# Kernel tuning notes

Hardware: AMD Instinct MI355X
Metric: run time of the kernel (lower is better)

Reference implementation:

```python
import jax, jax.numpy as jnp
import numpy as np

B, S, D, NB = 8, 8192, 512, 16


def _ln(x, g, b, eps=1e-5):
    m = jnp.mean(x, axis=-1, keepdims=True)
    v = jnp.var(x, axis=-1, keepdims=True)
    return (x - m) / jnp.sqrt(v + eps) * g + b


def setup_inputs() -> dict:
    key = jax.random.key(0)
    ks = jax.random.split(key, 12)
    s = 0.02
    f32 = jnp.float32
    return {
        "emb_input": jax.random.normal(ks[0], (B, S, D), f32),
        "dis_input": jax.random.normal(ks[1], (B, S, D), f32),
        "torsion": jax.random.normal(ks[2], (B, D), f32),
        "dis_unlocked": 1,
        "delay_steps": 3,
        # embodied selector + per-block params (stacked over NB blocks)
        "emb_sel_W": jax.random.normal(ks[3], (D, NB), f32) * s,
        "emb_sel_b": jnp.zeros((NB,), f32),
        "emb_ln_g": jnp.ones((NB, D), f32),
        "emb_ln_b": jnp.zeros((NB, D), f32),
        "emb_w1": jax.random.normal(ks[4], (NB, D, D), f32) * s,
        "emb_b1": jnp.zeros((NB, D), f32),
        "emb_w2": jax.random.normal(ks[5], (NB, D, D), f32) * s,
        "emb_b2": jnp.zeros((NB, D), f32),
        # disembodied selector + per-block params
        "dis_sel_W": jax.random.normal(ks[6], (D, NB), f32) * s,
        "dis_sel_b": jnp.zeros((NB,), f32),
        "dis_ln1_g": jnp.ones((NB, D), f32),
        "dis_ln1_b": jnp.zeros((NB, D), f32),
        "dis_attn_W": jax.random.normal(ks[7], (NB, D, D), f32) * s,
        "dis_attn_b": jnp.zeros((NB, D), f32),
        "dis_ln2_g": jnp.ones((NB, D), f32),
        "dis_ln2_b": jnp.zeros((NB, D), f32),
        "dis_ff1_W": jax.random.normal(ks[8], (NB, D, 2 * D), f32) * s,
        "dis_ff1_b": jnp.zeros((NB, 2 * D), f32),
        "dis_ff2_W": jax.random.normal(ks[9], (NB, 2 * D, D), f32) * s,
        "dis_ff2_b": jnp.zeros((NB, D), f32),
    }


def reference(emb_input, dis_input, torsion, dis_unlocked, delay_steps,
              emb_sel_W, emb_sel_b, emb_ln_g, emb_ln_b, emb_w1, emb_b1, emb_w2, emb_b2,
              dis_sel_W, dis_sel_b, dis_ln1_g, dis_ln1_b, dis_attn_W, dis_attn_b,
              dis_ln2_g, dis_ln2_b, dis_ff1_W, dis_ff1_b, dis_ff2_W, dis_ff2_b):
    # ---- embodied branch: sigmoid-gated top-2 routing (indices from batch elem 0)
    scores = jax.nn.sigmoid(jnp.mean(emb_input, axis=1) @ emb_sel_W + emb_sel_b)  # [B,NB]
    _, top = jax.lax.top_k(scores[0], 2)
    t_emb = 1.0 + torsion[:, None, :] * 0.1  # [B,1,D]
    h = emb_input
    for i in range(2):  # fixed top-2, unrolled; block params gathered dynamically
        idx = top[i]
        hn = _ln(h, emb_ln_g[idx], emb_ln_b[idx])
        hn = jnp.tanh(hn @ emb_w1[idx] + emb_b1[idx]) @ emb_w2[idx] + emb_b2[idx]
        h = h + hn * t_emb * 0.3
    emb_h = h

    # ---- disembodied branch (dis_unlocked is a static Python int)
    dis_h = None
    if dis_unlocked:
        delayed = jnp.mean(dis_input, axis=1)  # [B,D]; single-write buffer returns current mean
        dscores = jax.nn.sigmoid(delayed @ dis_sel_W + dis_sel_b)
        _, dtop = jax.lax.top_k(dscores[0], 2)
        t_dis = 1.0 + torsion[:, None, :] * 0.05
        dh = dis_input
        for i in range(2):
            idx = dtop[i]
            h1 = _ln(dh, dis_ln1_g[idx], dis_ln1_b[idx])
            h1 = h1 @ dis_attn_W[idx] + dis_attn_b[idx]
            h1 = (h1 + delayed[:, None, :] * 0.2) * t_dis
            hm = dh + h1 * 0.5
            h2 = _ln(hm, dis_ln2_g[idx], dis_ln2_b[idx])
            h2 = jax.nn.gelu(h2 @ dis_ff1_W[idx] + dis_ff1_b[idx], approximate=False)
            h2 = h2 @ dis_ff2_W[idx] + dis_ff2_b[idx]
            dh = hm + h2 * 0.5
        dis_h = dh
    return (emb_h, dis_h)
```

## Files before the change

kernel.cpp:

```cpp
#include <hip/hip_runtime.h>
#include <stdint.h>

#define B_  8
#define S_  8192
#define D_  512
#define NB_ 16
#define M_  (B_*S_)

typedef short bf16x8 __attribute__((ext_vector_type(8)));
typedef float f32x4  __attribute__((ext_vector_type(4)));

static __device__ __forceinline__ unsigned short f2bf(float f) {
  unsigned int u = __float_as_uint(f);
  u += 0x7fff + ((u >> 16) & 1);
  return (unsigned short)(u >> 16);
}

static __device__ __forceinline__ float fast_gelu(float v) {
  float x = fabsf(v) * 0.70710678118654752f;
  float t = __builtin_amdgcn_rcpf(1.f + 0.3275911f * x);
  float poly = ((((1.061405429f * t - 1.453152027f) * t + 1.421413741f) * t
                 - 0.284496736f) * t + 0.254829592f) * t;
  float erfx = 1.f - poly * __expf(-x * x);
  return 0.5f * v * (1.f + copysignf(erfx, v));
}

static __device__ __forceinline__ float fast_tanh(float v) {
  float a = fabsf(v);
  float e = __expf(2.f * a);
  float r = 1.f - 2.f * __builtin_amdgcn_rcpf(e + 1.f);
  return copysignf(r, v);
}

static __device__ __forceinline__ void async_copy16(const unsigned short* g,
                                                    unsigned short* l) {
  auto* g1 = reinterpret_cast<const __attribute__((address_space(1))) uint32_t*>(
      reinterpret_cast<uintptr_t>(g));
  auto* l3 = reinterpret_cast<__attribute__((address_space(3))) uint32_t*>(
      reinterpret_cast<uintptr_t>(l));
  __builtin_amdgcn_global_load_lds(g1, l3, 16, 0, 0);
}

__global__ __launch_bounds__(256) void zero_kernel(float* p, int n) {
  int i = blockIdx.x * 256 + threadIdx.x;
  if (i < n) p[i] = 0.f;
}

__global__ __launch_bounds__(512) void colmean_kernel(const float* __restrict__ x,
                                                      float* __restrict__ acc) {
  int b = blockIdx.x, d = threadIdx.x;
  const float* p = x + ((size_t)b * S_ + (size_t)blockIdx.y * 512) * D_ + d;
  float s = 0.f;
  #pragma unroll 8
  for (int i = 0; i < 512; i++) s += p[(size_t)i * D_];
  atomicAdd(&acc[b * D_ + d], s);
}

__global__ __launch_bounds__(128) void top2_kernel(const float* __restrict__ embAcc,
                                                   const float* __restrict__ embW,
                                                   const float* __restrict__ embB,
                                                   const float* __restrict__ disAcc,
                                                   const float* __restrict__ disW,
                                                   const float* __restrict__ disB,
                                                   int* __restrict__ out) {
  int wave = threadIdx.x >> 6, lane = threadIdx.x & 63;
  const float* acc = wave ? disAcc : embAcc;
  const float* W   = wave ? disW   : embW;
  const float* bb  = wave ? disB   : embB;
  const float invS = 1.f / (float)S_;
  float logit[NB_];
  for (int nb = 0; nb < NB_; nb++) {
    float s = 0.f;
    for (int d = lane; d < D_; d += 64) s += acc[d] * invS * W[d * NB_ + nb];
    for (int o = 32; o; o >>= 1) s += __shfl_xor(s, o);
    logit[nb] = s + bb[nb];
  }
  if (lane == 0) {
    int i0 = 0;
    for (int i = 1; i < NB_; i++) if (logit[i] > logit[i0]) i0 = i;
    int i1 = (i0 == 0) ? 1 : 0;
    for (int i = 0; i < NB_; i++) if (i != i0 && logit[i] > logit[i1]) i1 = i;
    out[wave * 2 + 0] = i0;
    out[wave * 2 + 1] = i1;
  }
}

__global__ __launch_bounds__(256) void ln_cast_kernel(const float* __restrict__ x,
                                                      const float* __restrict__ gB,
                                                      const float* __restrict__ bB,
                                                      const int* __restrict__ idxPtr,
                                                      unsigned short* __restrict__ out) {
  int row  = blockIdx.x * 4 + (threadIdx.x >> 6);
  int lane = threadIdx.x & 63;
  const float4* xr = (const float4*)(x + (size_t)row * D_ + lane * 8);
  float4 v0 = xr[0], v1 = xr[1];
  float s  = v0.x + v0.y + v0.z + v0.w + v1.x + v1.y + v1.z + v1.w;
  float sq = v0.x*v0.x + v0.y*v0.y + v0.z*v0.z + v0.w*v0.w
           + v1.x*v1.x + v1.y*v1.y + v1.z*v1.z + v1.w*v1.w;
  for (int o = 32; o; o >>= 1) { s += __shfl_xor(s, o); sq += __shfl_xor(sq, o); }
  float mean = s * (1.f / D_);
  float var  = sq * (1.f / D_) - mean * mean;
  float rstd = rsqrtf(var + 1e-5f);
  int idx = *idxPtr;
  const float4* g4 = (const float4*)(gB + (size_t)idx * D_ + lane * 8);
  const float4* b4 = (const float4*)(bB + (size_t)idx * D_ + lane * 8);
  float4 g0 = g4[0], g1 = g4[1], c0 = b4[0], c1 = b4[1];
  float xv[8] = {v0.x, v0.y, v0.z, v0.w, v1.x, v1.y, v1.z, v1.w};
  float gv[8] = {g0.x, g0.y, g0.z, g0.w, g1.x, g1.y, g1.z, g1.w};
  float bv[8] = {c0.x, c0.y, c0.z, c0.w, c1.x, c1.y, c1.z, c1.w};
  unsigned short o8[8] __attribute__((aligned(16)));
  #pragma unroll
  for (int k = 0; k < 8; k++) o8[k] = f2bf((xv[k] - mean) * rstd * gv[k] + bv[k]);
  *(uint4*)(out + (size_t)row * D_ + lane * 8) = *(const uint4*)o8;
}

__global__ __launch_bounds__(256) void wconvert_kernel(const float* __restrict__ srcAll,
                                                       const int* __restrict__ idxPtr,
                                                       int K, int N,
                                                       unsigned short* __restrict__ dst) {
  __shared__ float t[32][33];
  int idx = *idxPtr;
  const float* src = srcAll + (size_t)idx * K * N;
  int k0 = blockIdx.y * 32, n0 = blockIdx.x * 32;
  int tid = threadIdx.x;
  int kl = tid >> 5, nl = tid & 31;
  #pragma unroll
  for (int r = 0; r < 4; r++)
    t[kl + r * 8][nl] = src[(size_t)(k0 + kl + r * 8) * N + n0 + nl];
  __syncthreads();
  #pragma unroll
  for (int r = 0; r < 4; r++)
    dst[(size_t)(n0 + kl + r * 8) * K + k0 + nl] = f2bf(t[nl][kl + r * 8]);
}

template<int EPI>
__global__ __launch_bounds__(256, 3) void gemm_kernel(const unsigned short* __restrict__ A,
                                                      const unsigned short* __restrict__ Bt,
                                                      int K, int N,
                                                      const int* __restrict__ idxPtr,
                                                      const float* __restrict__ biasBase,
                                                      const float* __restrict__ hin,
                                                      float* __restrict__ fout,
                                                      unsigned short* __restrict__ bout,
                                                      const float* __restrict__ torsion,
                                                      const float* __restrict__ dAcc) {
  __shared__ __align__(16) unsigned short lds[3][2][4096];
  const int tid  = threadIdx.x;
  const int wid  = tid >> 6, lane = tid & 63;
  const int quad = lane >> 4, l16 = lane & 15;
  const int wm = (wid >> 1) * 64, wn = (wid & 1) * 64;

  const int nT  = N >> 7;
  const int lgn = (nT == 4) ? 2 : 3;
  const int perX = gridDim.x >> 3;
  const int tile = ((int)blockIdx.x & 7) * perX + ((int)blockIdx.x >> 3);
  const int m0 = (tile >> lgn) << 7;
  const int n0 = (tile & (nT - 1)) << 7;

  const int srow = tid >> 2;
  const int scol = (((tid & 3) ^ ((tid >> 3) & 3)) * 8);
  const unsigned short* Ag0 = A  + (size_t)(m0 + srow) * K + scol;
  const unsigned short* Ag1 = Ag0 + (size_t)64 * K;
  const unsigned short* Bg0 = Bt + (size_t)(n0 + srow) * K + scol;
  const unsigned short* Bg1 = Bg0 + (size_t)64 * K;

  auto stage = [&](int kt, int slot) {
    async_copy16(Ag0 + (size_t)kt * 32, &lds[slot][0][tid * 8]);
    async_copy16(Ag1 + (size_t)kt * 32, &lds[slot][0][2048 + tid * 8]);
    async_copy16(Bg0 + (size_t)kt * 32, &lds[slot][1][tid * 8]);
    async_copy16(Bg1 + (size_t)kt * 32, &lds[slot][1][2048 + tid * 8]);
  };

  f32x4 acc[4][4] = {};
  const int nK = K >> 5;

  stage(0, 0);
  stage(1, 1);

  const int rsw  = (l16 >> 1) & 3;
  const int aoff = (wm + l16) * 32 + ((quad ^ rsw) * 8);
  const int boff = (wn + l16) * 32 + ((quad ^ rsw) * 8);

  for (int k = 0; k < nK; ++k) {
    const int cur = k % 3;
    const int nxt = (k + 2) % 3;
    const int kn  = (k + 2 < nK) ? (k + 2) : 0;
    stage(kn, nxt);
    asm volatile("s_waitcnt vmcnt(8)" ::: "memory");
    asm volatile("s_barrier" ::: "memory");

    const unsigned short* Ab = &lds[cur][0][aoff];
    const unsigned short* Bb = &lds[cur][1][boff];
    bf16x8 af[4], bfr[4];
    #pragma unroll
    for (int i = 0; i < 4; ++i) af[i]  = *(const bf16x8*)(Ab + i * 512);
    #pragma unroll
    for (int j = 0; j < 4; ++j) bfr[j] = *(const bf16x8*)(Bb + j * 512);
    __builtin_amdgcn_s_setprio(1);
    #pragma unroll
    for (int i = 0; i < 4; ++i)
      #pragma unroll
      for (int j = 0; j < 4; ++j)
        acc[i][j] = __builtin_amdgcn_mfma_f32_16x16x32_bf16(af[i], bfr[j], acc[i][j], 0, 0, 0);
    __builtin_amdgcn_s_setprio(0);
    asm volatile("s_barrier" ::: "memory");
  }

  const int idx = *idxPtr;
  const float* bias = biasBase + (size_t)idx * N;
  const float invS = 1.f / (float)S_;
  #pragma unroll
  for (int i = 0; i < 4; ++i) {
    int rowb = m0 + wm + i * 16 + quad * 4;
    #pragma unroll
    for (int j = 0; j < 4; ++j) {
      int col = n0 + wn + j * 16 + l16;
      float bc = bias[col];
      #pragma unroll
      for (int r = 0; r < 4; ++r) {
        int row = rowb + r;
        size_t off = (size_t)row * N + col;
        float v = acc[i][j][r] + bc;
        if constexpr (EPI == 0) {
          bout[off] = f2bf(fast_tanh(v));
        } else if constexpr (EPI == 1) {
          int b = row >> 13;
          float t = 1.f + 0.1f * torsion[b * D_ + col];
          fout[off] = hin[off] + v * t * 0.3f;
        } else if constexpr (EPI == 2) {
          int b = row >> 13;
          float t = 1.f + 0.05f * torsion[b * D_ + col];
          float h1 = (v + 0.2f * dAcc[b * D_ + col] * invS) * t;
          fout[off] = hin[off] + 0.5f * h1;
        } else if constexpr (EPI == 3) {
          bout[off] = f2bf(fast_gelu(v));
        } else {
          fout[off] = hin[off] + 0.5f * v;
        }
      }
    }
  }
  asm volatile("s_waitcnt vmcnt(0)" ::: "memory");
}

extern "C" void kernel_launch(void* const* d_in, const int* in_sizes, int n_in,
                              void* d_out, int out_size, void* d_ws, size_t ws_size,
                              hipStream_t stream) {
  const float* emb_input  = (const float*)d_in[0];
  const float* dis_input  = (const float*)d_in[1];
  const float* torsion    = (const float*)d_in[2];
  const float* emb_sel_W  = (const float*)d_in[5];
  const float* emb_sel_b  = (const float*)d_in[6];
  const float* emb_ln_g   = (const float*)d_in[7];
  const float* emb_ln_b   = (const float*)d_in[8];
  const float* emb_w1     = (const float*)d_in[9];
  const float* emb_b1     = (const float*)d_in[10];
  const float* emb_w2     = (const float*)d_in[11];
  const float* emb_b2     = (const float*)d_in[12];
  const float* dis_sel_W  = (const float*)d_in[13];
  const float* dis_sel_b  = (const float*)d_in[14];
  const float* dis_ln1_g  = (const float*)d_in[15];
  const float* dis_ln1_b  = (const float*)d_in[16];
  const float* dis_attn_W = (const float*)d_in[17];
  const float* dis_attn_b = (const float*)d_in[18];
  const float* dis_ln2_g  = (const float*)d_in[19];
  const float* dis_ln2_b  = (const float*)d_in[20];
  const float* dis_ff1_W  = (const float*)d_in[21];
  const float* dis_ff1_b  = (const float*)d_in[22];
  const float* dis_ff2_W  = (const float*)d_in[23];
  const float* dis_ff2_b  = (const float*)d_in[24];

  char* w = (char*)d_ws;
  float* accE = (float*)w;
  float* accD = (float*)(w + 16384);
  int*   top  = (int*)(w + 32768);
  size_t o = 33024;
  unsigned short* w1t   = (unsigned short*)(w + o); o += 524288;
  unsigned short* w2t   = (unsigned short*)(w + o); o += 524288;
  unsigned short* attnT = (unsigned short*)(w + o); o += 524288;
  unsigned short* ff1T  = (unsigned short*)(w + o); o += 1048576;
  unsigned short* ff2T  = (unsigned short*)(w + o); o += 1048576;
  unsigned short* Abuf  = (unsigned short*)(w + o); o += (size_t)M_ * D_ * 2;
  unsigned short* T1    = (unsigned short*)(w + o); o += (size_t)M_ * D_ * 2;

  float* outEmb = (float*)d_out;
  float* outDis = outEmb + (size_t)M_ * D_;
  unsigned short* Gbuf = (unsigned short*)d_out;

  zero_kernel<<<32, 256, 0, stream>>>(accE, 2 * B_ * D_);
  colmean_kernel<<<dim3(1, 16), 512, 0, stream>>>(emb_input, accE);
  colmean_kernel<<<dim3(8, 16), 512, 0, stream>>>(dis_input, accD);
  top2_kernel<<<1, 128, 0, stream>>>(accE, emb_sel_W, emb_sel_b,
                                     accD, dis_sel_W, dis_sel_b, top);

  for (int s = 0; s < 2; s++) {
    const int* di = top + 2 + s;
    const float* dh = (s == 0) ? dis_input : outDis;
    wconvert_kernel<<<dim3(16, 16), 256, 0, stream>>>(dis_attn_W, di, 512, 512, attnT);
    wconvert_kernel<<<dim3(32, 16), 256, 0, stream>>>(dis_ff1_W,  di, 512, 1024, ff1T);
    wconvert_kernel<<<dim3(16, 32), 256, 0, stream>>>(dis_ff2_W,  di, 1024, 512, ff2T);
    ln_cast_kernel<<<M_ / 4, 256, 0, stream>>>(dh, dis_ln1_g, dis_ln1_b, di, Abuf);
    gemm_kernel<2><<<2048, 256, 0, stream>>>(Abuf, attnT, 512, 512, di,
        dis_attn_b, dh, outDis, nullptr, torsion, accD);
    ln_cast_kernel<<<M_ / 4, 256, 0, stream>>>(outDis, dis_ln2_g, dis_ln2_b, di, Abuf);
    gemm_kernel<3><<<4096, 256, 0, stream>>>(Abuf, ff1T, 512, 1024, di,
        dis_ff1_b, nullptr, nullptr, Gbuf, nullptr, nullptr);
    gemm_kernel<4><<<2048, 256, 0, stream>>>(Gbuf, ff2T, 1024, 512, di,
        dis_ff2_b, outDis, outDis, nullptr, nullptr, nullptr);
  }

  for (int s = 0; s < 2; s++) {
    const int* ei = top + s;
    const float* h = (s == 0) ? emb_input : outEmb;
    wconvert_kernel<<<dim3(16, 16), 256, 0, stream>>>(emb_w1, ei, 512, 512, w1t);
    wconvert_kernel<<<dim3(16, 16), 256, 0, stream>>>(emb_w2, ei, 512, 512, w2t);
    ln_cast_kernel<<<M_ / 4, 256, 0, stream>>>(h, emb_ln_g, emb_ln_b, ei, Abuf);
    gemm_kernel<0><<<2048, 256, 0, stream>>>(Abuf, w1t, 512, 512, ei,
        emb_b1, nullptr, nullptr, T1, nullptr, nullptr);
    gemm_kernel<1><<<2048, 256, 0, stream>>>(T1, w2t, 512, 512, ei,
        emb_b2, h, outEmb, nullptr, torsion, nullptr);
  }
}
```

Measured before the change: 1.598 ms.

## Use 8-wave 512-thread GEMM blocks with 64x32 warp tiles and peeled pipeline

The GEMM kernel now runs 512 threads (8 waves) per 128x128 tile instead of 256, so each wave computes a 64x32 sub-tile and each thread issues one async copy for A and one for B per stage. The K loop is restructured so the tail is peeled, with explicit vmcnt values and a fixed ring index instead of modulo, which removes the dummy prefetch of tile 0. Epilogue bias, torsion and delayed-mean loads are hoisted out of the row loop. The aim is more waves in flight to hide latency and fewer accumulator registers per wave, at the cost of more barrier participants and fewer MFMAs per LDS fragment load.

```diff
diff --git a/kernel.cpp b/kernel.cpp
--- a/kernel.cpp
+++ b/kernel.cpp
@@ -134,7 +134,7 @@
 }
 
 template<int EPI>
-__global__ __launch_bounds__(256, 3) void gemm_kernel(const unsigned short* __restrict__ A,
+__global__ __launch_bounds__(512, 6) void gemm_kernel(const unsigned short* __restrict__ A,
                                                       const unsigned short* __restrict__ Bt,
                                                       int K, int N,
                                                       const int* __restrict__ idxPtr,
@@ -144,11 +144,11 @@
                                                       unsigned short* __restrict__ bout,
                                                       const float* __restrict__ torsion,
                                                       const float* __restrict__ dAcc) {
-  __shared__ __align__(16) unsigned short lds[3][2][4096];
+  __shared__ __align__(16) unsigned short ring[3][2][4096];
   const int tid  = threadIdx.x;
   const int wid  = tid >> 6, lane = tid & 63;
   const int quad = lane >> 4, l16 = lane & 15;
-  const int wm = (wid >> 1) * 64, wn = (wid & 1) * 64;
+  const int wr = wid >> 2, wc = wid & 3;
 
   const int nT  = N >> 7;
   const int lgn = (nT == 4) ? 2 : 3;
@@ -159,79 +159,86 @@
 
   const int srow = tid >> 2;
   const int scol = (((tid & 3) ^ ((tid >> 3) & 3)) * 8);
-  const unsigned short* Ag0 = A  + (size_t)(m0 + srow) * K + scol;
-  const unsigned short* Ag1 = Ag0 + (size_t)64 * K;
-  const unsigned short* Bg0 = Bt + (size_t)(n0 + srow) * K + scol;
-  const unsigned short* Bg1 = Bg0 + (size_t)64 * K;
+  const unsigned short* Ag = A  + (size_t)(m0 + srow) * K + scol;
+  const unsigned short* Bg = Bt + (size_t)(n0 + srow) * K + scol;
 
   auto stage = [&](int kt, int slot) {
-    async_copy16(Ag0 + (size_t)kt * 32, &lds[slot][0][tid * 8]);
-    async_copy16(Ag1 + (size_t)kt * 32, &lds[slot][0][2048 + tid * 8]);
-    async_copy16(Bg0 + (size_t)kt * 32, &lds[slot][1][tid * 8]);
-    async_copy16(Bg1 + (size_t)kt * 32, &lds[slot][1][2048 + tid * 8]);
+    async_copy16(Ag + (size_t)kt * 32, &ring[slot][0][tid * 8]);
+    async_copy16(Bg + (size_t)kt * 32, &ring[slot][1][tid * 8]);
   };
 
-  f32x4 acc[4][4] = {};
+  f32x4 acc[4][2] = {};
   const int nK = K >> 5;
 
   stage(0, 0);
   stage(1, 1);
 
   const int rsw  = (l16 >> 1) & 3;
-  const int aoff = (wm + l16) * 32 + ((quad ^ rsw) * 8);
-  const int boff = (wn + l16) * 32 + ((quad ^ rsw) * 8);
-
-  for (int k = 0; k < nK; ++k) {
-    const int cur = k % 3;
-    const int nxt = (k + 2) % 3;
-    const int kn  = (k + 2 < nK) ? (k + 2) : 0;
-    stage(kn, nxt);
-    asm volatile("s_waitcnt vmcnt(8)" ::: "memory");
-    asm volatile("s_barrier" ::: "memory");
-
-    const unsigned short* Ab = &lds[cur][0][aoff];
-    const unsigned short* Bb = &lds[cur][1][boff];
-    bf16x8 af[4], bfr[4];
-    #pragma unroll
-    for (int i = 0; i < 4; ++i) af[i]  = *(const bf16x8*)(Ab + i * 512);
-    #pragma unroll
-    for (int j = 0; j < 4; ++j) bfr[j] = *(const bf16x8*)(Bb + j * 512);
-    __builtin_amdgcn_s_setprio(1);
-    #pragma unroll
-    for (int i = 0; i < 4; ++i)
-      #pragma unroll
-      for (int j = 0; j < 4; ++j)
-        acc[i][j] = __builtin_amdgcn_mfma_f32_16x16x32_bf16(af[i], bfr[j], acc[i][j], 0, 0, 0);
-    __builtin_amdgcn_s_setprio(0);
-    asm volatile("s_barrier" ::: "memory");
-  }
+  const int aoff = (wr * 64 + l16) * 32 + ((quad ^ rsw) * 8);
+  const int boff = (wc * 32 + l16) * 32 + ((quad ^ rsw) * 8);
+
+#define KSTEP(CUR, VM) do {                                                     \
+    asm volatile("s_waitcnt vmcnt(" VM ")" ::: "memory");                       \
+    asm volatile("s_barrier" ::: "memory");                                     \
+    const unsigned short* Ab = &ring[(CUR)][0][0] + aoff;                       \
+    const unsigned short* Bb = &ring[(CUR)][1][0] + boff;                       \
+    bf16x8 af[4], bfr[2];                                                       \
+    _Pragma("unroll")                                                           \
+    for (int i_ = 0; i_ < 4; ++i_) af[i_]  = *(const bf16x8*)(Ab + i_ * 512);   \
+    _Pragma("unroll")                                                           \
+    for (int j_ = 0; j_ < 2; ++j_) bfr[j_] = *(const bf16x8*)(Bb + j_ * 512);   \
+    __builtin_amdgcn_s_setprio(1);                                              \
+    _Pragma("unroll")                                                           \
+    for (int i_ = 0; i_ < 4; ++i_)                                              \
+      _Pragma("unroll")                                                         \
+      for (int j_ = 0; j_ < 2; ++j_)                                            \
+        acc[i_][j_] = __builtin_amdgcn_mfma_f32_16x16x32_bf16(af[i_], bfr[j_],  \
+                                                              acc[i_][j_], 0, 0, 0); \
+    __builtin_amdgcn_s_setprio(0);                                              \
+    asm volatile("s_barrier" ::: "memory");                                     \
+  } while (0)
+
+  int cur = 0, nxt = 2;
+  for (int k = 0; k + 2 < nK; ++k) {
+    stage(k + 2, nxt);
+    KSTEP(cur, "4");
+    cur = (cur == 2) ? 0 : cur + 1;
+    nxt = (nxt == 2) ? 0 : nxt + 1;
+  }
+  KSTEP(cur, "2");
+  cur = (cur == 2) ? 0 : cur + 1;
+  KSTEP(cur, "0");
+#undef KSTEP
 
   const int idx = *idxPtr;
   const float* bias = biasBase + (size_t)idx * N;
+  const int bcn = m0 >> 13;
   const float invS = 1.f / (float)S_;
+  float bc[2], tv[2], dv[2];
+  #pragma unroll
+  for (int j = 0; j < 2; ++j) {
+    int col = n0 + wc * 32 + j * 16 + l16;
+    bc[j] = bias[col];
+    if constexpr (EPI == 1) tv[j] = 1.f + 0.1f  * torsion[bcn * D_ + col];
+    if constexpr (EPI == 2) tv[j] = 1.f + 0.05f * torsion[bcn * D_ + col];
+    if constexpr (EPI == 2) dv[j] = 0.2f * dAcc[bcn * D_ + col] * invS;
+  }
   #pragma unroll
   for (int i = 0; i < 4; ++i) {
-    int rowb = m0 + wm + i * 16 + quad * 4;
+    int rowb = m0 + wr * 64 + i * 16 + quad * 4;
     #pragma unroll
-    for (int j = 0; j < 4; ++j) {
-      int col = n0 + wn + j * 16 + l16;
-      float bc = bias[col];
+    for (int j = 0; j < 2; ++j) {
+      int col = n0 + wc * 32 + j * 16 + l16;
       #pragma unroll
       for (int r = 0; r < 4; ++r) {
-        int row = rowb + r;
-        size_t off = (size_t)row * N + col;
-        float v = acc[i][j][r] + bc;
+        size_t off = (size_t)(rowb + r) * N + col;
+        float v = acc[i][j][r] + bc[j];
         if constexpr (EPI == 0) {
           bout[off] = f2bf(fast_tanh(v));
         } else if constexpr (EPI == 1) {
-          int b = row >> 13;
-          float t = 1.f + 0.1f * torsion[b * D_ + col];
-          fout[off] = hin[off] + v * t * 0.3f;
+          fout[off] = hin[off] + v * tv[j] * 0.3f;
         } else if constexpr (EPI == 2) {
-          int b = row >> 13;
-          float t = 1.f + 0.05f * torsion[b * D_ + col];
-          float h1 = (v + 0.2f * dAcc[b * D_ + col] * invS) * t;
-          fout[off] = hin[off] + 0.5f * h1;
+          fout[off] = hin[off] + 0.5f * ((v + dv[j]) * tv[j]);
         } else if constexpr (EPI == 3) {
           bout[off] = f2bf(fast_gelu(v));
         } else {
@@ -240,7 +247,6 @@
       }
     }
   }
-  asm volatile("s_waitcnt vmcnt(0)" ::: "memory");
 }
 
 extern "C" void kernel_launch(void* const* d_in, const int* in_sizes, int n_in,
@@ -300,12 +306,12 @@
     wconvert_kernel<<<dim3(32, 16), 256, 0, stream>>>(dis_ff1_W,  di, 512, 1024, ff1T);
     wconvert_kernel<<<dim3(16, 32), 256, 0, stream>>>(dis_ff2_W,  di, 1024, 512, ff2T);
     ln_cast_kernel<<<M_ / 4, 256, 0, stream>>>(dh, dis_ln1_g, dis_ln1_b, di, Abuf);
-    gemm_kernel<2><<<2048, 256, 0, stream>>>(Abuf, attnT, 512, 512, di,
+    gemm_kernel<2><<<2048, 512, 0, stream>>>(Abuf, attnT, 512, 512, di,
         dis_attn_b, dh, outDis, nullptr, torsion, accD);
     ln_cast_kernel<<<M_ / 4, 256, 0, stream>>>(outDis, dis_ln2_g, dis_ln2_b, di, Abuf);
-    gemm_kernel<3><<<4096, 256, 0, stream>>>(Abuf, ff1T, 512, 1024, di,
+    gemm_kernel<3><<<4096, 512, 0, stream>>>(Abuf, ff1T, 512, 1024, di,
         dis_ff1_b, nullptr, nullptr, Gbuf, nullptr, nullptr);
-    gemm_kernel<4><<<2048, 256, 0, stream>>>(Gbuf, ff2T, 1024, 512, di,
+    gemm_kernel<4><<<2048, 512, 0, stream>>>(Gbuf, ff2T, 1024, 512, di,
         dis_ff2_b, outDis, outDis, nullptr, nullptr, nullptr);
   }
 
@@ -315,9 +321,9 @@
     wconvert_kernel<<<dim3(16, 16), 256, 0, stream>>>(emb_w1, ei, 512, 512, w1t);
     wconvert_kernel<<<dim3(16, 16), 256, 0, stream>>>(emb_w2, ei, 512, 512, w2t);
     ln_cast_kernel<<<M_ / 4, 256, 0, stream>>>(h, emb_ln_g, emb_ln_b, ei, Abuf);
-    gemm_kernel<0><<<2048, 256, 0, stream>>>(Abuf, w1t, 512, 512, ei,
+    gemm_kernel<0><<<2048, 512, 0, stream>>>(Abuf, w1t, 512, 512, ei,
         emb_b1, nullptr, nullptr, T1, nullptr, nullptr);
-    gemm_kernel<1><<<2048, 256, 0, stream>>>(T1, w2t, 512, 512, ei,
+    gemm_kernel<1><<<2048, 512, 0, stream>>>(T1, w2t, 512, 512, ei,
         emb_b2, h, outEmb, nullptr, torsion, nullptr);
   }
 }
```

After: 1.581 ms. Within noise of the previous version (-1.1%).
